# Kernel optimization log

Hardware: AMD Instinct MI355X
Metric: run time of the kernel (lower is better)

Reference implementation:

```python
import jax, jax.numpy as jnp
import numpy as np

N_T = 2_000_000      # terrain nodes
E_SEQ = 2_000_000    # sequence edges
E_AS = 2_000_000     # assignment edges
N_TOR = 1_000_000    # torus nodes
E_TR = 8_000_000     # transport edges
TD, OD, PD, N_OPS = 4, 3, 1, 4  # terrain dim, torus dim, polarity dim, num operators


def setup_inputs() -> dict:
    key = jax.random.key(0)
    ks = jax.random.split(key, 12)
    inp = {
        "x_terrain": jax.random.normal(ks[0], (N_T, TD), jnp.float32),
        "polarity": jax.random.normal(ks[1], (E_AS, PD), jnp.float32),
        "x_torus": jax.random.normal(ks[2], (N_TOR, OD), jnp.float32),
        "seq_ei": jax.random.randint(ks[3], (2, E_SEQ), 0, N_T),
        "assign_src": jax.random.randint(ks[4], (E_AS,), 0, N_T),
        "assign_dst": jax.random.randint(ks[5], (E_AS,), 0, N_OPS),
        "tr_ei": jax.random.randint(ks[6], (2, E_TR), 0, N_TOR),
        # learned params (nn.Linear convention: y = x @ W.T + b)
        "W_seq": jax.random.normal(ks[7], (TD, TD), jnp.float32) * 0.5,      # SequenceConv.lin, no bias
        "op_W": jax.random.normal(ks[8], (N_OPS, TD, TD + PD), jnp.float32) * 0.4,
        "op_b": jax.random.normal(ks[9], (N_OPS, TD), jnp.float32) * 0.1,
        "gate_W": jax.random.normal(ks[10], (2 * OD, 1), jnp.float32) * 0.4,  # TransportConv.gate
        "gate_b": jax.random.normal(ks[11], (1,), jnp.float32) * 0.1,
    }
    return inp


def _engine_fwd(x_terrain, polarity, x_torus, W_seq, op_W, op_b, gate_W, gate_b,
                seq_ei, assign_src, assign_dst, tr_ei):
    # 1) SequenceConv: add-aggregated linear message along terrain cycle, residual add
    msg = x_terrain[seq_ei[0]] @ W_seq.T                       # [E_seq, TD]
    agg = jnp.zeros_like(x_terrain).at[seq_ei[1]].add(msg)     # scatter-add to dst
    x_t = x_terrain + agg

    # 2) per-node operator transform: first assignment edge per source node
    E = assign_src.shape[0]
    pos = jnp.arange(E, dtype=jnp.int32)
    first = jax.ops.segment_min(pos, assign_src, num_segments=x_t.shape[0])  # fill = int32 max
    has = first < E                                            # nodes with >=1 assignment
    fe = jnp.clip(first, 0, E - 1)
    op_idx = jnp.clip(assign_dst[fe], 0, op_W.shape[0] - 1)    # [N_T]
    pol = polarity[fe]                                         # [N_T, 1]
    inp = jnp.concatenate([x_t, pol], axis=-1)                 # [N_T, TD+1]
    out = jnp.einsum('nij,nj->ni', op_W[op_idx], inp) + op_b[op_idx]
    x_t = jnp.where(has[:, None], out, x_t)

    # 3) TransportConv: sigmoid-gated mean aggregation over torus edges, residual add
    src, dst = tr_ei[0], tr_ei[1]
    xi, xj = x_torus[dst], x_torus[src]
    gate = jax.nn.sigmoid(jnp.concatenate([xi, xj], axis=-1) @ gate_W + gate_b)  # [E_tr,1]
    m = gate * xj
    s = jax.ops.segment_sum(m, dst, num_segments=x_torus.shape[0])
    cnt = jax.ops.segment_sum(jnp.ones((m.shape[0],), m.dtype), dst,
                              num_segments=x_torus.shape[0])
    x_tor = x_torus + s / jnp.maximum(cnt, 1.0)[:, None]
    return x_t, x_tor


def reference(x_terrain, polarity, x_torus, seq_ei, assign_src, assign_dst, tr_ei,
              W_seq, op_W, op_b, gate_W, gate_b):
    return _engine_fwd(x_terrain, polarity, x_torus, W_seq, op_W, op_b, gate_W, gate_b,
                       seq_ei, assign_src, assign_dst, tr_ei)
```

## Files before the change

### kernel.cpp

```cpp
#include <hip/hip_runtime.h>
#include <hip/hip_fp16.h>
#include <math.h>

#define N_T   2000000
#define E_SEQ 2000000
#define E_AS  2000000
#define N_TOR 1000000
#define E_TR  8000000

typedef unsigned long long u64;

__device__ __forceinline__ long long center_field(u64 t, int bits) {
    long long h = 1LL << (bits - 1);
    return (long long)((t & ((1ULL << bits) - 1)) ^ (u64)h) - h;
}

#define INIT_U64S ((size_t)N_T * 2 + N_TOR)
__global__ __launch_bounds__(256) void init_kernel(ulonglong2* __restrict__ ws) {
    size_t i = (size_t)blockIdx.x * blockDim.x + threadIdx.x;
    if (i >= INIT_U64S / 2) return;
    size_t idx64 = i * 2;
    u64 v = (idx64 >= (size_t)N_T && idx64 < (size_t)2 * N_T) ? ~0ULL : 0ULL;
    ws[i] = make_ulonglong2(v, v);
}

__global__ __launch_bounds__(256) void prep_kernel(
        const float* __restrict__ x_torus,
        const float* __restrict__ gate_W,
        const float* __restrict__ gate_b,
        float4* __restrict__ src_f4,
        float* __restrict__ yi_arr) {
    int n = blockIdx.x * blockDim.x + threadIdx.x;
    if (n >= N_TOR) return;
    const float* x = x_torus + (size_t)n * 3;
    float x0 = x[0], x1 = x[1], x2 = x[2];
    float yi = fmaf(x0, gate_W[0], fmaf(x1, gate_W[1], x2 * gate_W[2]));
    float yj = fmaf(x0, gate_W[3], fmaf(x1, gate_W[4], fmaf(x2, gate_W[5], gate_b[0])));
    src_f4[n] = make_float4(x0, x1, x2, yj);
    yi_arr[n] = yi;
}

__global__ __launch_bounds__(256) void edge_kernel(
        const float4* __restrict__ src_f4,
        const float* __restrict__ yi_arr,
        const int* __restrict__ tr_src,
        const int* __restrict__ tr_dst,
        u64* __restrict__ tor_pk,
        const float4* __restrict__ x_terrain,
        const int* __restrict__ seq_src,
        const int* __restrict__ seq_dst,
        const float* __restrict__ W_seq,
        u64* __restrict__ agg_pk,
        const int* __restrict__ assign_src,
        const int* __restrict__ assign_dst,
        const float* __restrict__ polarity,
        u64* __restrict__ first_pk) {
    int i = blockIdx.x * blockDim.x + threadIdx.x;
    if (i < E_TR) {
        int e = i;
        int si = __builtin_nontemporal_load(tr_src + e);
        int di = __builtin_nontemporal_load(tr_dst + e);
        float4 s = src_f4[si];
        float z = yi_arr[di] + s.w;
        float g = 1.0f / (1.0f + __expf(-z));
        long long f0 = __float2int_rn(g * s.x * 128.0f);
        long long f1 = __float2int_rn(g * s.y * 128.0f);
        long long f2 = __float2int_rn(g * s.z * 128.0f);
        long long pk = f0 + (f1 << 17) + (f2 << 34) + (1LL << 51);
        atomicAdd(&tor_pk[di], (u64)pk);
    } else if (i < E_TR + E_SEQ) {
        int e = i - E_TR;
        int s = __builtin_nontemporal_load(seq_src + e);
        int d = __builtin_nontemporal_load(seq_dst + e);
        float4 x = x_terrain[s];
        float m0 = fmaf(x.x, W_seq[0],  fmaf(x.y, W_seq[1],  fmaf(x.z, W_seq[2],  x.w * W_seq[3])));
        float m1 = fmaf(x.x, W_seq[4],  fmaf(x.y, W_seq[5],  fmaf(x.z, W_seq[6],  x.w * W_seq[7])));
        float m2 = fmaf(x.x, W_seq[8],  fmaf(x.y, W_seq[9],  fmaf(x.z, W_seq[10], x.w * W_seq[11])));
        float m3 = fmaf(x.x, W_seq[12], fmaf(x.y, W_seq[13], fmaf(x.z, W_seq[14], x.w * W_seq[15])));
        long long f0 = __float2int_rn(m0 * 256.0f);
        long long f1 = __float2int_rn(m1 * 256.0f);
        long long f2 = __float2int_rn(m2 * 256.0f);
        long long f3 = __float2int_rn(m3 * 256.0f);
        long long pk = f0 + (f1 << 16) + (f2 << 32) + (f3 << 48);
        atomicAdd(&agg_pk[d], (u64)pk);
    } else if (i < E_TR + E_SEQ + E_AS) {
        int e = i - (E_TR + E_SEQ);
        int op = __builtin_nontemporal_load(assign_dst + e) & 3;
        __half h = __float2half(__builtin_nontemporal_load(polarity + e));
        unsigned short hb;
        __builtin_memcpy(&hb, &h, 2);
        u64 key = ((u64)e << 18) | ((u64)op << 16) | (u64)hb;
        atomicMin(&first_pk[__builtin_nontemporal_load(assign_src + e)], key);
    }
}

__global__ __launch_bounds__(256) void node_kernel(
        const float4* __restrict__ x_terrain,
        const u64* __restrict__ agg_pk,
        const u64* __restrict__ first_pk,
        const float* __restrict__ op_W,
        const float* __restrict__ op_b,
        float4* __restrict__ out_xt,
        const float* __restrict__ x_torus,
        const u64* __restrict__ tor_pk,
        float* __restrict__ out_tor) {
    int i = blockIdx.x * blockDim.x + threadIdx.x;
    if (i < N_T) {
        int n = i;
        float4 x = x_terrain[n];
        u64 t = agg_pk[n];
        long long m0 = center_field(t, 16); t = (t - (u64)m0) >> 16;
        long long m1 = center_field(t, 16); t = (t - (u64)m1) >> 16;
        long long m2 = center_field(t, 16); t = (t - (u64)m2) >> 16;
        long long m3 = center_field(t, 16);
        const float inv = 1.0f / 256.0f;
        x.x += (float)m0 * inv; x.y += (float)m1 * inv;
        x.z += (float)m2 * inv; x.w += (float)m3 * inv;
        u64 fp = first_pk[n];
        if ((fp >> 18) < (u64)E_AS) {
            int op = (int)((fp >> 16) & 3);
            unsigned short hb = (unsigned short)(fp & 0xFFFF);
            __half h;
            __builtin_memcpy(&h, &hb, 2);
            float pol = __half2float(h);
            const float* W = op_W + op * 20;
            const float* b = op_b + op * 4;
            float4 o;
            o.x = fmaf(x.x, W[0],  fmaf(x.y, W[1],  fmaf(x.z, W[2],  fmaf(x.w, W[3],  fmaf(pol, W[4],  b[0])))));
            o.y = fmaf(x.x, W[5],  fmaf(x.y, W[6],  fmaf(x.z, W[7],  fmaf(x.w, W[8],  fmaf(pol, W[9],  b[1])))));
            o.z = fmaf(x.x, W[10], fmaf(x.y, W[11], fmaf(x.z, W[12], fmaf(x.w, W[13], fmaf(pol, W[14], b[2])))));
            o.w = fmaf(x.x, W[15], fmaf(x.y, W[16], fmaf(x.z, W[17], fmaf(x.w, W[18], fmaf(pol, W[19], b[3])))));
            x = o;
        }
        out_xt[n] = x;
    } else if (i < N_T + N_TOR) {
        int n = i - N_T;
        u64 t = tor_pk[n];
        long long m0 = center_field(t, 17); t = (t - (u64)m0) >> 17;
        long long m1 = center_field(t, 17); t = (t - (u64)m1) >> 17;
        long long m2 = center_field(t, 17); t = (t - (u64)m2) >> 17;
        float cnt = (float)(t & 0x1FFF);
        float inv = (1.0f / 128.0f) / fmaxf(cnt, 1.0f);
        size_t b = (size_t)n * 3;
        out_tor[b + 0] = x_torus[b + 0] + (float)m0 * inv;
        out_tor[b + 1] = x_torus[b + 1] + (float)m1 * inv;
        out_tor[b + 2] = x_torus[b + 2] + (float)m2 * inv;
    }
}

extern "C" void kernel_launch(void* const* d_in, const int* in_sizes, int n_in,
                              void* d_out, int out_size, void* d_ws, size_t ws_size,
                              hipStream_t stream) {
    const float* x_terrain  = (const float*)d_in[0];
    const float* polarity   = (const float*)d_in[1];
    const float* x_torus    = (const float*)d_in[2];
    const int*   seq_ei     = (const int*)  d_in[3];
    const int*   assign_src = (const int*)  d_in[4];
    const int*   assign_dst = (const int*)  d_in[5];
    const int*   tr_ei      = (const int*)  d_in[6];
    const float* W_seq      = (const float*)d_in[7];
    const float* op_W       = (const float*)d_in[8];
    const float* op_b       = (const float*)d_in[9];
    const float* gate_W     = (const float*)d_in[10];
    const float* gate_b     = (const float*)d_in[11];

    float* out_xt  = (float*)d_out;
    float* out_tor = (float*)d_out + (size_t)N_T * 4;

    char* ws = (char*)d_ws;
    u64* agg_pk   = (u64*)ws;
    u64* first_pk = agg_pk + N_T;
    u64* tor_pk   = first_pk + N_T;

    float4* src_f4 = (float4*)d_out;
    float*  yi_arr = (float*)d_out + (size_t)N_TOR * 4;

    const int B = 256;
    const long long init_v2 = (long long)(INIT_U64S / 2);
    init_kernel<<<(int)((init_v2 + B - 1) / B), B, 0, stream>>>((ulonglong2*)ws);
    prep_kernel<<<(N_TOR + B - 1) / B, B, 0, stream>>>(x_torus, gate_W, gate_b,
                                                       src_f4, yi_arr);

    const long long total_e = (long long)E_TR + E_SEQ + E_AS;
    edge_kernel<<<(int)((total_e + B - 1) / B), B, 0, stream>>>(
        src_f4, yi_arr, tr_ei, tr_ei + E_TR, tor_pk,
        (const float4*)x_terrain, seq_ei, seq_ei + E_SEQ, W_seq, agg_pk,
        assign_src, assign_dst, polarity, first_pk);
    const long long total_n = (long long)N_T + N_TOR;
    node_kernel<<<(int)((total_n + B - 1) / B), B, 0, stream>>>(
        (const float4*)x_terrain, agg_pk, first_pk, op_W, op_b, (float4*)out_xt,
        x_torus, tor_pk, out_tor);
}
```

Measured before the change: 700.1 us.

## Replicate torus accumulators per XCD with workgroup-scope atomics, then reduce

Torus edge atomics now go to one of 8 per-XCD replica arrays, chosen by the hardware XCC id and issued with workgroup-scope atomics, so they stay in each die's local L2 and avoid cross-die coherence traffic. A reduce kernel then sums the replicas. Source node features are packed to fp16 in a single u64, and the transport edges are split from the seq/assign edges into separate kernels with workspace reuse. In exchange it adds extra kernels, replica memory traffic, and fp16 rounding of the inputs. It also relies on workgroup-scope atomics behaving correctly across CUs that share an XCD.

```diff
diff --git a/kernel.cpp b/kernel.cpp
--- a/kernel.cpp
+++ b/kernel.cpp
@@ -7,6 +7,7 @@
 #define E_AS  2000000
 #define N_TOR 1000000
 #define E_TR  8000000
+#define NREP  8
 
 typedef unsigned long long u64;
 
@@ -15,61 +16,93 @@
     return (long long)((t & ((1ULL << bits) - 1)) ^ (u64)h) - h;
 }
 
-#define INIT_U64S ((size_t)N_T * 2 + N_TOR)
-__global__ __launch_bounds__(256) void init_kernel(ulonglong2* __restrict__ ws) {
-    size_t i = (size_t)blockIdx.x * blockDim.x + threadIdx.x;
-    if (i >= INIT_U64S / 2) return;
-    size_t idx64 = i * 2;
-    u64 v = (idx64 >= (size_t)N_T && idx64 < (size_t)2 * N_T) ? ~0ULL : 0ULL;
-    ws[i] = make_ulonglong2(v, v);
+__device__ __forceinline__ unsigned xcc_id() {
+    return __builtin_amdgcn_s_getreg((3 << 11) | 20) & 7u;
+}
+
+__global__ __launch_bounds__(256) void initA_kernel(ulonglong2* __restrict__ a,
+                                                    ulonglong2* __restrict__ b) {
+    long long i = (long long)blockIdx.x * blockDim.x + threadIdx.x;
+    if (i < 2500000LL) a[i] = make_ulonglong2(0, 0);
+    else if (i < 4000000LL) b[i - 2500000LL] = make_ulonglong2(0, 0);
 }
 
 __global__ __launch_bounds__(256) void prep_kernel(
         const float* __restrict__ x_torus,
-        const float* __restrict__ gate_W,
-        const float* __restrict__ gate_b,
-        float4* __restrict__ src_f4,
-        float* __restrict__ yi_arr) {
+        const float* __restrict__ gate_W, const float* __restrict__ gate_b,
+        u64* __restrict__ src_pk, float* __restrict__ yi_arr) {
     int n = blockIdx.x * blockDim.x + threadIdx.x;
     if (n >= N_TOR) return;
     const float* x = x_torus + (size_t)n * 3;
     float x0 = x[0], x1 = x[1], x2 = x[2];
     float yi = fmaf(x0, gate_W[0], fmaf(x1, gate_W[1], x2 * gate_W[2]));
     float yj = fmaf(x0, gate_W[3], fmaf(x1, gate_W[4], fmaf(x2, gate_W[5], gate_b[0])));
-    src_f4[n] = make_float4(x0, x1, x2, yj);
+    unsigned short u0, u1, u2, u3;
+    __half h;
+    h = __float2half(x0); __builtin_memcpy(&u0, &h, 2);
+    h = __float2half(x1); __builtin_memcpy(&u1, &h, 2);
+    h = __float2half(x2); __builtin_memcpy(&u2, &h, 2);
+    h = __float2half(yj); __builtin_memcpy(&u3, &h, 2);
+    src_pk[n] = (u64)u0 | ((u64)u1 << 16) | ((u64)u2 << 32) | ((u64)u3 << 48);
     yi_arr[n] = yi;
 }
 
-__global__ __launch_bounds__(256) void edge_kernel(
-        const float4* __restrict__ src_f4,
-        const float* __restrict__ yi_arr,
-        const int* __restrict__ tr_src,
-        const int* __restrict__ tr_dst,
-        u64* __restrict__ tor_pk,
+__global__ __launch_bounds__(256) void tr_kernel(
+        const int* __restrict__ tr_src, const int* __restrict__ tr_dst,
+        const u64* __restrict__ src_pk, const float* __restrict__ yi_arr,
+        u64* rep_ws, u64* rep_out) {
+    int e = blockIdx.x * blockDim.x + threadIdx.x;
+    if (e >= E_TR) return;
+    int si = __builtin_nontemporal_load(tr_src + e);
+    int di = __builtin_nontemporal_load(tr_dst + e);
+    u64 s = __builtin_nontemporal_load(src_pk + si);
+    unsigned short u0 = (unsigned short)s, u1 = (unsigned short)(s >> 16),
+                   u2 = (unsigned short)(s >> 32), u3 = (unsigned short)(s >> 48);
+    __half h0, h1, h2, h3;
+    __builtin_memcpy(&h0, &u0, 2); __builtin_memcpy(&h1, &u1, 2);
+    __builtin_memcpy(&h2, &u2, 2); __builtin_memcpy(&h3, &u3, 2);
+    float x0 = __half2float(h0), x1 = __half2float(h1), x2 = __half2float(h2);
+    float z = yi_arr[di] + __half2float(h3);
+    float g = 1.0f / (1.0f + __expf(-z));
+    long long f0 = __float2int_rn(g * x0 * 128.0f);
+    long long f1 = __float2int_rn(g * x1 * 128.0f);
+    long long f2 = __float2int_rn(g * x2 * 128.0f);
+    long long pk = f0 + (f1 << 17) + (f2 << 34) + (1LL << 51);
+    unsigned r = xcc_id();
+    u64* rep = (r < 5) ? rep_ws + (size_t)r * N_TOR
+                       : rep_out + (size_t)(r - 5) * N_TOR;
+    __hip_atomic_fetch_add(&rep[di], (u64)pk, __ATOMIC_RELAXED,
+                           __HIP_MEMORY_SCOPE_WORKGROUP);
+}
+
+__global__ __launch_bounds__(256) void reduce_kernel(
+        const u64* rep_ws, const u64* rep_out, u64* tor_sum) {
+    int n = blockIdx.x * blockDim.x + threadIdx.x;
+    if (n >= N_TOR) return;
+    u64 t = 0;
+    #pragma unroll
+    for (int r = 0; r < 5; ++r) t += rep_ws[(size_t)r * N_TOR + n];
+    #pragma unroll
+    for (int r = 0; r < 3; ++r) t += rep_out[(size_t)r * N_TOR + n];
+    tor_sum[n] = t;
+}
+
+__global__ __launch_bounds__(256) void initB_kernel(ulonglong2* __restrict__ ws) {
+    long long i = (long long)blockIdx.x * blockDim.x + threadIdx.x;
+    if (i >= 2000000LL) return;
+    u64 v = (i * 2 < (long long)N_T) ? 0ULL : ~0ULL;
+    ws[i] = make_ulonglong2(v, v);
+}
+
+__global__ __launch_bounds__(256) void sa_kernel(
         const float4* __restrict__ x_terrain,
-        const int* __restrict__ seq_src,
-        const int* __restrict__ seq_dst,
-        const float* __restrict__ W_seq,
-        u64* __restrict__ agg_pk,
-        const int* __restrict__ assign_src,
-        const int* __restrict__ assign_dst,
-        const float* __restrict__ polarity,
-        u64* __restrict__ first_pk) {
+        const int* __restrict__ seq_src, const int* __restrict__ seq_dst,
+        const float* __restrict__ W_seq, u64* __restrict__ agg_pk,
+        const int* __restrict__ assign_src, const int* __restrict__ assign_dst,
+        const float* __restrict__ polarity, u64* __restrict__ first_pk) {
     int i = blockIdx.x * blockDim.x + threadIdx.x;
-    if (i < E_TR) {
+    if (i < E_SEQ) {
         int e = i;
-        int si = __builtin_nontemporal_load(tr_src + e);
-        int di = __builtin_nontemporal_load(tr_dst + e);
-        float4 s = src_f4[si];
-        float z = yi_arr[di] + s.w;
-        float g = 1.0f / (1.0f + __expf(-z));
-        long long f0 = __float2int_rn(g * s.x * 128.0f);
-        long long f1 = __float2int_rn(g * s.y * 128.0f);
-        long long f2 = __float2int_rn(g * s.z * 128.0f);
-        long long pk = f0 + (f1 << 17) + (f2 << 34) + (1LL << 51);
-        atomicAdd(&tor_pk[di], (u64)pk);
-    } else if (i < E_TR + E_SEQ) {
-        int e = i - E_TR;
         int s = __builtin_nontemporal_load(seq_src + e);
         int d = __builtin_nontemporal_load(seq_dst + e);
         float4 x = x_terrain[s];
@@ -83,8 +116,8 @@
         long long f3 = __float2int_rn(m3 * 256.0f);
         long long pk = f0 + (f1 << 16) + (f2 << 32) + (f3 << 48);
         atomicAdd(&agg_pk[d], (u64)pk);
-    } else if (i < E_TR + E_SEQ + E_AS) {
-        int e = i - (E_TR + E_SEQ);
+    } else if (i < E_SEQ + E_AS) {
+        int e = i - E_SEQ;
         int op = __builtin_nontemporal_load(assign_dst + e) & 3;
         __half h = __float2half(__builtin_nontemporal_load(polarity + e));
         unsigned short hb;
@@ -98,11 +131,10 @@
         const float4* __restrict__ x_terrain,
         const u64* __restrict__ agg_pk,
         const u64* __restrict__ first_pk,
-        const float* __restrict__ op_W,
-        const float* __restrict__ op_b,
+        const float* __restrict__ op_W, const float* __restrict__ op_b,
         float4* __restrict__ out_xt,
         const float* __restrict__ x_torus,
-        const u64* __restrict__ tor_pk,
+        const u64* __restrict__ tor_sum,
         float* __restrict__ out_tor) {
     int i = blockIdx.x * blockDim.x + threadIdx.x;
     if (i < N_T) {
@@ -135,7 +167,7 @@
         out_xt[n] = x;
     } else if (i < N_T + N_TOR) {
         int n = i - N_T;
-        u64 t = tor_pk[n];
+        u64 t = tor_sum[n];
         long long m0 = center_field(t, 17); t = (t - (u64)m0) >> 17;
         long long m1 = center_field(t, 17); t = (t - (u64)m1) >> 17;
         long long m2 = center_field(t, 17); t = (t - (u64)m2) >> 17;
@@ -167,27 +199,30 @@
     float* out_xt  = (float*)d_out;
     float* out_tor = (float*)d_out + (size_t)N_T * 4;
 
-    char* ws = (char*)d_ws;
-    u64* agg_pk   = (u64*)ws;
-    u64* first_pk = agg_pk + N_T;
-    u64* tor_pk   = first_pk + N_T;
-
-    float4* src_f4 = (float4*)d_out;
-    float*  yi_arr = (float*)d_out + (size_t)N_TOR * 4;
+    u64* wsu      = (u64*)d_ws;
+    u64* rep_ws   = wsu;
+    u64* agg_pk   = wsu;
+    u64* first_pk = wsu + N_T;
+    u64* tor_sum  = wsu + 2 * (size_t)N_T;
+    u64* rep_out  = (u64*)d_out;
+    u64* src_pk   = (u64*)d_out + 3 * (size_t)N_TOR;
+    float* yi_arr = (float*)((u64*)d_out + 4 * (size_t)N_TOR);
 
     const int B = 256;
-    const long long init_v2 = (long long)(INIT_U64S / 2);
-    init_kernel<<<(int)((init_v2 + B - 1) / B), B, 0, stream>>>((ulonglong2*)ws);
-    prep_kernel<<<(N_TOR + B - 1) / B, B, 0, stream>>>(x_torus, gate_W, gate_b,
-                                                       src_f4, yi_arr);
-
-    const long long total_e = (long long)E_TR + E_SEQ + E_AS;
-    edge_kernel<<<(int)((total_e + B - 1) / B), B, 0, stream>>>(
-        src_f4, yi_arr, tr_ei, tr_ei + E_TR, tor_pk,
+    initA_kernel<<<(4000000 + B - 1) / B, B, 0, stream>>>(
+        (ulonglong2*)rep_ws, (ulonglong2*)rep_out);
+    prep_kernel<<<(N_TOR + B - 1) / B, B, 0, stream>>>(
+        x_torus, gate_W, gate_b, src_pk, yi_arr);
+    tr_kernel<<<(E_TR + B - 1) / B, B, 0, stream>>>(
+        tr_ei, tr_ei + E_TR, src_pk, yi_arr, rep_ws, rep_out);
+    reduce_kernel<<<(N_TOR + B - 1) / B, B, 0, stream>>>(
+        rep_ws, rep_out, tor_sum);
+    initB_kernel<<<(2000000 + B - 1) / B, B, 0, stream>>>((ulonglong2*)wsu);
+    sa_kernel<<<((E_SEQ + E_AS) + B - 1) / B, B, 0, stream>>>(
         (const float4*)x_terrain, seq_ei, seq_ei + E_SEQ, W_seq, agg_pk,
         assign_src, assign_dst, polarity, first_pk);
     const long long total_n = (long long)N_T + N_TOR;
     node_kernel<<<(int)((total_n + B - 1) / B), B, 0, stream>>>(
         (const float4*)x_terrain, agg_pk, first_pk, op_W, op_b, (float4*)out_xt,
-        x_torus, tor_pk, out_tor);
-}
+        x_torus, tor_sum, out_tor);
+}
```

Result: slower. 737.6 us (+5.4%).
